# Kernel optimization log

Measured on AMD Instinct MI355X. Metric: run time of the kernel, lower is better.

The kernel has to match this reference:

```python
import jax, jax.numpy as jnp
import numpy as np

DIM = 2048
DIM_HEAD = 128
HEADS = 16
FF_MULT = 4
ATTN_INNER = DIM_HEAD * HEADS            # 2048
FF_INNER = DIM * FF_MULT                 # 8192
FUSED_OUT = ATTN_INNER + 2 * DIM_HEAD + 2 * FF_INNER  # 18688
EPS = 1e-5


def setup_inputs() -> dict:
    key = jax.random.key(0)
    ks = jax.random.split(key, 5)
    B, N = 1, 2048
    x = jax.random.normal(ks[0], (B, N, DIM), dtype=jnp.float32)
    gamma = jnp.ones((DIM,), dtype=jnp.float32)
    # store weights as [in, out] for x @ W
    w_fused = jax.random.normal(ks[1], (DIM, FUSED_OUT), dtype=jnp.float32) * (DIM ** -0.5)
    w_attn_out = jax.random.normal(ks[2], (ATTN_INNER, DIM), dtype=jnp.float32) * (ATTN_INNER ** -0.5)
    w_ff_out = jax.random.normal(ks[3], (FF_INNER, DIM), dtype=jnp.float32) * (FF_INNER ** -0.5)
    return {"x": x, "gamma": gamma, "w_fused": w_fused,
            "w_attn_out": w_attn_out, "w_ff_out": w_ff_out}


def reference(x, gamma, w_fused, w_attn_out, w_ff_out):
    b, n, d = x.shape
    h, dh = HEADS, DIM_HEAD
    scale = dh ** -0.5

    # LayerNorm (beta fixed at 0)
    mu = jnp.mean(x, axis=-1, keepdims=True)
    var = jnp.mean(jnp.square(x - mu), axis=-1, keepdims=True)
    xn = (x - mu) * jax.lax.rsqrt(var + EPS) * gamma

    # fused QKV + FF projection
    proj = xn @ w_fused  # [b, n, FUSED_OUT]
    q = proj[..., :ATTN_INNER]
    k = proj[..., ATTN_INNER:ATTN_INNER + dh]
    v = proj[..., ATTN_INNER + dh:ATTN_INNER + 2 * dh]
    ff = proj[..., ATTN_INNER + 2 * dh:]

    # multi-query attention: q per-head, k/v shared
    q = q.reshape(b, n, h, dh).transpose(0, 2, 1, 3) * scale  # [b,h,n,dh]
    sim = jnp.einsum('bhid,bjd->bhij', q, k)
    causal = jnp.triu(jnp.ones((n, n), dtype=bool), k=1)
    neg = -jnp.finfo(sim.dtype).max
    sim = jnp.where(causal, neg, sim)
    attn = jax.nn.softmax(sim, axis=-1)
    out = jnp.einsum('bhij,bjd->bhid', attn, v)
    out = out.transpose(0, 2, 1, 3).reshape(b, n, h * dh)
    attn_out = out @ w_attn_out

    # parallel SwiGLU FFN
    ff_x, gate = jnp.split(ff, 2, axis=-1)
    ff_out = (jax.nn.silu(gate) * ff_x) @ w_ff_out

    return attn_out + ff_out
```

## Files before the change

kernel.cpp:

```cpp
#include <hip/hip_runtime.h>
#include <hip/hip_bf16.h>

typedef unsigned short u16;
typedef __bf16 bf16x8 __attribute__((ext_vector_type(8)));
typedef float f32x4 __attribute__((ext_vector_type(4)));

#define DIM 2048
#define SEQ 2048
#define HEADS 16
#define DH 128
#define FUSED_OUT 18688
#define FF_INNER 8192
#define KOFF 2048
#define VOFF 2176
#define FFOFF 2304
#define AE_LD 10240

#define WS_XN   0
#define WS_WFT  8388608
#define WS_PROJ 84934656
#define WS_VT   161480704
#define WS_BTE  0
#define WS_AE   41943040

__device__ __forceinline__ float b2f(u16 u) {
  union { unsigned int i; float f; } c; c.i = ((unsigned int)u) << 16; return c.f;
}
__device__ __forceinline__ u16 f2b(float f) {
  union { float f; unsigned int i; } c; c.f = f;
  return (u16)((c.i + 0x7fffu + ((c.i >> 16) & 1u)) >> 16);
}
__device__ __forceinline__ void async16(void* lds, const void* g) {
  __builtin_amdgcn_global_load_lds((const __attribute__((address_space(1))) unsigned int*)g,
                                   (__attribute__((address_space(3))) unsigned int*)lds,
                                   16, 0, 0);
}

union U8 { uint4 v; u16 s[8]; };

__global__ void __launch_bounds__(256) ln_kernel(const float* __restrict__ x,
                                                 const float* __restrict__ gamma,
                                                 u16* __restrict__ xn) {
  const int row = blockIdx.x, tid = threadIdx.x;
  const int lane = tid & 63, wv = tid >> 6;
  float v[8], s1 = 0.f, s2 = 0.f;
  {
    float4 a0 = *(const float4*)(x + (size_t)row * DIM + tid * 8);
    float4 a1 = *(const float4*)(x + (size_t)row * DIM + tid * 8 + 4);
    v[0] = a0.x; v[1] = a0.y; v[2] = a0.z; v[3] = a0.w;
    v[4] = a1.x; v[5] = a1.y; v[6] = a1.z; v[7] = a1.w;
  }
#pragma unroll
  for (int i = 0; i < 8; ++i) { s1 += v[i]; s2 += v[i] * v[i]; }
#pragma unroll
  for (int off = 32; off > 0; off >>= 1) {
    s1 += __shfl_down(s1, off, 64);
    s2 += __shfl_down(s2, off, 64);
  }
  __shared__ float r1[4], r2[4];
  if (lane == 0) { r1[wv] = s1; r2[wv] = s2; }
  __syncthreads();
  s1 = r1[0] + r1[1] + r1[2] + r1[3];
  s2 = r2[0] + r2[1] + r2[2] + r2[3];
  const float inv = 1.0f / DIM;
  const float mu = s1 * inv;
  const float var = s2 * inv - mu * mu;
  const float rs = rsqrtf(var + 1e-5f);
  float4 g0 = *(const float4*)(gamma + tid * 8);
  float4 g1 = *(const float4*)(gamma + tid * 8 + 4);
  const float gm[8] = {g0.x, g0.y, g0.z, g0.w, g1.x, g1.y, g1.z, g1.w};
  U8 o;
#pragma unroll
  for (int i = 0; i < 8; ++i) o.s[i] = f2b((v[i] - mu) * rs * gm[i]);
  *(uint4*)(xn + (size_t)row * DIM + tid * 8) = o.v;
}

__global__ void __launch_bounds__(256) transpose_f2b64(const float* __restrict__ in,
                                                       u16* __restrict__ out,
                                                       int ldin, int ldout) {
  __shared__ u16 t[64][65];
  const int tx = threadIdx.x, ty = threadIdx.y;
  const int r0 = blockIdx.y * 64, c0 = blockIdx.x * 64;
#pragma unroll
  for (int i = 0; i < 16; ++i)
    t[ty + i * 4][tx] = f2b(in[(size_t)(r0 + ty + i * 4) * ldin + c0 + tx]);
  __syncthreads();
#pragma unroll
  for (int i = 0; i < 16; ++i)
    out[(size_t)(c0 + ty + i * 4) * ldout + r0 + tx] = t[tx][ty + i * 4];
}

__global__ void __launch_bounds__(256) trans_wout64(const float* __restrict__ w_attn,
                                                    const float* __restrict__ w_ff,
                                                    u16* __restrict__ BtE) {
  __shared__ u16 t[64][65];
  const int tx = threadIdx.x, ty = threadIdx.y;
  const int c0 = blockIdx.x * 64;
  const float* in; int r0, kout;
  if (blockIdx.y < 32) { in = w_attn; r0 = blockIdx.y * 64; kout = r0; }
  else { in = w_ff; r0 = (blockIdx.y - 32) * 64; kout = 2048 + r0; }
#pragma unroll
  for (int i = 0; i < 16; ++i)
    t[ty + i * 4][tx] = f2b(in[(size_t)(r0 + ty + i * 4) * DIM + c0 + tx]);
  __syncthreads();
#pragma unroll
  for (int i = 0; i < 16; ++i)
    BtE[(size_t)(c0 + ty + i * 4) * AE_LD + kout + tx] = t[tx][ty + i * 4];
}

__global__ void __launch_bounds__(256) transpose_u16_64(const u16* __restrict__ in,
                                                        u16* __restrict__ out,
                                                        int ldin, int ldout) {
  __shared__ u16 t[64][65];
  const int tx = threadIdx.x, ty = threadIdx.y;
  const int r0 = blockIdx.y * 64, c0 = blockIdx.x * 64;
#pragma unroll
  for (int i = 0; i < 16; ++i)
    t[ty + i * 4][tx] = in[(size_t)(r0 + ty + i * 4) * ldin + c0 + tx];
  __syncthreads();
#pragma unroll
  for (int i = 0; i < 16; ++i)
    out[(size_t)(c0 + ty + i * 4) * ldout + r0 + tx] = t[tx][ty + i * 4];
}

#define BAR()    asm volatile("s_barrier" ::: "memory")
#define LGKM0()  asm volatile("s_waitcnt lgkmcnt(0)" ::: "memory")
#define RA(mi, kk) (*(const bf16x8*)&sA[c][(wm * 128 + (mi) * 16 + lhalf) * 64 + ((((kk) * 4 + lgrp) ^ key) << 3)])
#define RB(ni, kk) (*(const bf16x8*)&sB[c][(wn * 64 + (ni) * 16 + lhalf) * 64 + ((((kk) * 4 + lgrp) ^ key) << 3)])
#define MFMA_Q(MB, AA)                                                   \
  _Pragma("unroll") for (int kk = 0; kk < 2; ++kk)                       \
  _Pragma("unroll") for (int u = 0; u < 2; ++u)                          \
  _Pragma("unroll") for (int ni = 0; ni < 4; ++ni)                       \
      acc[(MB) + u][ni] = __builtin_amdgcn_mfma_f32_16x16x32_bf16(       \
          AA[u][kk], bF[ni][kk], acc[(MB) + u][ni], 0, 0, 0);

__device__ __forceinline__ void stage_h(u16* lds, const u16* g, int ld,
                                        int wv, int srow, int scol) {
  async16(lds + wv * 512,        g + (size_t)(wv * 8 + srow) * ld + scol);
  async16(lds + 4096 + wv * 512, g + (size_t)(64 + wv * 8 + srow) * ld + scol);
}

template <int OUTMODE>
__global__ void __launch_bounds__(512, 2) gemm8p(const u16* __restrict__ A,
                                                 const u16* __restrict__ Bt,
                                                 void* __restrict__ Cv,
                                                 int Ksz, int lda, int ldb, int ldc) {
  __shared__ alignas(16) u16 sA[2][256 * 64];
  __shared__ alignas(16) u16 sB[2][256 * 64];
  const int tid = threadIdx.x;
  const int lane = tid & 63, wv = tid >> 6;
  const int wm = wv >> 2, wn = wv & 3;
  const int lhalf = lane & 15, lgrp = lane >> 4;
  const int key = lhalf & 7;
  const int srow = lane >> 3;
  const int scol = ((lane & 7) ^ srow) << 3;
  const int m0 = blockIdx.x * 256, n0 = blockIdx.y * 256;
  const int kbeg = blockIdx.z * Ksz;
  const int NT = Ksz >> 6;

  const u16* Abase = A + (size_t)m0 * lda + kbeg;
  const u16* Bbase = Bt + (size_t)n0 * ldb + kbeg;

  stage_h(&sB[0][0],    Bbase,                     ldb, wv, srow, scol);
  stage_h(&sB[0][8192], Bbase + (size_t)128 * ldb, ldb, wv, srow, scol);
  stage_h(&sA[0][0],    Abase,                     lda, wv, srow, scol);
  stage_h(&sA[0][8192], Abase + (size_t)128 * lda, lda, wv, srow, scol);
  asm volatile("s_waitcnt vmcnt(4)" ::: "memory");
  stage_h(&sB[1][0],    Bbase + 64,                     ldb, wv, srow, scol);
  stage_h(&sB[1][8192], Bbase + (size_t)128 * ldb + 64, ldb, wv, srow, scol);
  stage_h(&sA[1][0],    Abase + 64,                     lda, wv, srow, scol);
  asm volatile("s_waitcnt vmcnt(6)" ::: "memory");
  BAR();

  f32x4 acc[8][4];
  const f32x4 fzero = {0.f, 0.f, 0.f, 0.f};
#pragma unroll
  for (int i = 0; i < 8; ++i)
#pragma unroll
    for (int j = 0; j < 4; ++j) acc[i][j] = fzero;

  bf16x8 bF[4][2];
  bf16x8 aF[2][2];
  bf16x8 aX[2][2];

  int t1w = 1;
  int t2w = 2 % NT;
  for (int t = 0; t < NT; ++t) {
    const int c = t & 1;
#pragma unroll
    for (int kk = 0; kk < 2; ++kk) {
      aF[0][kk] = RA(0, kk); aF[1][kk] = RA(1, kk);
#pragma unroll
      for (int ni = 0; ni < 4; ++ni) bF[ni][kk] = RB(ni, kk);
    }
    stage_h(&sA[c ^ 1][8192], Abase + (size_t)128 * lda + t1w * 64, lda, wv, srow, scol);
    asm volatile("s_waitcnt lgkmcnt(8)" ::: "memory");
    BAR(); LGKM0();
    __builtin_amdgcn_s_setprio(1);
    MFMA_Q(0, aF);
    __builtin_amdgcn_s_setprio(0);
    BAR();
#pragma unroll
    for (int kk = 0; kk < 2; ++kk) { aF[0][kk] = RA(2, kk); aF[1][kk] = RA(3, kk); }
    stage_h(&sB[c][0], Bbase + t2w * 64, ldb, wv, srow, scol);
    BAR(); LGKM0();
    __builtin_amdgcn_s_setprio(1);
    MFMA_Q(2, aF);
    __builtin_amdgcn_s_setprio(0);
    BAR();
#pragma unroll
    for (int kk = 0; kk < 2; ++kk) { aF[0][kk] = RA(4, kk); aF[1][kk] = RA(5, kk); }
    if (wm == 0) {
#pragma unroll
      for (int kk = 0; kk < 2; ++kk) { aX[0][kk] = RA(6, kk); aX[1][kk] = RA(7, kk); }
    }
    stage_h(&sB[c][8192], Bbase + (size_t)128 * ldb + t2w * 64, ldb, wv, srow, scol);
    BAR(); LGKM0();
    __builtin_amdgcn_s_setprio(1);
    MFMA_Q(4, aF);
    __builtin_amdgcn_s_setprio(0);
    BAR();
    if (wm != 0) {
#pragma unroll
      for (int kk = 0; kk < 2; ++kk) { aF[0][kk] = RA(6, kk); aF[1][kk] = RA(7, kk); }
    }
    stage_h(&sA[c][0], Abase + t2w * 64, lda, wv, srow, scol);
    asm volatile("s_waitcnt vmcnt(6)" ::: "memory");
    BAR(); LGKM0();
    __builtin_amdgcn_s_setprio(1);
    if (wm == 0) { MFMA_Q(6, aX); } else { MFMA_Q(6, aF); }
    __builtin_amdgcn_s_setprio(0);
    BAR();
    t1w = (t1w + 1 == NT) ? 0 : t1w + 1;
    t2w = (t2w + 1 == NT) ? 0 : t2w + 1;
  }
  asm volatile("s_waitcnt vmcnt(0)" ::: "memory");
#pragma unroll
  for (int mi = 0; mi < 8; ++mi)
#pragma unroll
    for (int ni = 0; ni < 4; ++ni)
#pragma unroll
      for (int tt = 0; tt < 4; ++tt) {
        const int row = m0 + wm * 128 + mi * 16 + lgrp * 4 + tt;
        const int col = n0 + wn * 64 + ni * 16 + lhalf;
        if (OUTMODE == 0) ((u16*)Cv)[(size_t)row * ldc + col] = f2b(acc[mi][ni][tt]);
        else atomicAdd((float*)Cv + (size_t)row * ldc + col, acc[mi][ni][tt]);
      }
}

__global__ void __launch_bounds__(256) attn_kernel(const u16* __restrict__ proj,
                                                   const u16* __restrict__ Vt,
                                                   u16* __restrict__ Ae) {
  const int h = blockIdx.y, qi = blockIdx.x;
  const int tid = threadIdx.x;
  const int lane = tid & 63, wv = tid >> 6;
  const int lhalf = lane & 15, lgrp = lane >> 4;
  const int key = lhalf & 7;

  __shared__ alignas(16) u16 Ks[128 * 128];
  __shared__ alignas(16) u16 Vts[128 * 128];
  __shared__ alignas(16) u16 Ps[4][16 * 128];

  const int sr = lane >> 4;
  const int sb = lane & 15;

  bf16x8 aq[4];
  {
    const u16* gq = proj + (size_t)(qi * 64 + wv * 16 + lhalf) * FUSED_OUT + h * DH;
#pragma unroll
    for (int kk = 0; kk < 4; ++kk) aq[kk] = *(const bf16x8*)(gq + kk * 32 + lgrp * 8);
  }
  const f32x4 fzero = {0.f, 0.f, 0.f, 0.f};
  f32x4 o[8];
#pragma unroll
  for (int i = 0; i < 8; ++i) o[i] = fzero;
  float mrow[4] = {-__builtin_inff(), -__builtin_inff(), -__builtin_inff(), -__builtin_inff()};
  float lrow[4] = {0.f, 0.f, 0.f, 0.f};
  const float scale = 0.088388347648318447f;
  const int jmax = (qi * 64 + 63) >> 7;

  for (int jt = 0; jt <= jmax; ++jt) {
    __syncthreads();
#pragma unroll
    for (int i = 0; i < 8; ++i) {
      const int ch = wv * 8 + i;
      const int row = ch * 4 + sr;
      const int gb = sb ^ (row & 7);
      async16(&Ks[ch * 512], proj + (size_t)(jt * 128 + row) * FUSED_OUT + KOFF + gb * 8);
      async16(&Vts[ch * 512], Vt + (size_t)row * SEQ + jt * 128 + gb * 8);
    }
    __syncthreads();
    f32x4 s[8];
#pragma unroll
    for (int sub = 0; sub < 8; ++sub) {
      f32x4 a = fzero;
#pragma unroll
      for (int kk = 0; kk < 4; ++kk) {
        bf16x8 bk = *(const bf16x8*)&Ks[(sub * 16 + lhalf) * 128 + (((kk * 4 + lgrp) ^ key) << 3)];
        a = __builtin_amdgcn_mfma_f32_16x16x32_bf16(aq[kk], bk, a, 0, 0, 0);
      }
      s[sub] = a;
    }
    const int row_g = qi * 64 + wv * 16 + lgrp * 4;
    const int col_b = jt * 128 + lhalf;
#pragma unroll
    for (int t = 0; t < 4; ++t) {
      float mx = -__builtin_inff();
#pragma unroll
      for (int sub = 0; sub < 8; ++sub) {
        float v = s[sub][t] * scale;
        if (col_b + sub * 16 > row_g + t) v = -__builtin_inff();
        s[sub][t] = v;
        mx = fmaxf(mx, v);
      }
      mx = fmaxf(mx, __shfl_xor(mx, 1, 64));
      mx = fmaxf(mx, __shfl_xor(mx, 2, 64));
      mx = fmaxf(mx, __shfl_xor(mx, 4, 64));
      mx = fmaxf(mx, __shfl_xor(mx, 8, 64));
      const float mnew = fmaxf(mrow[t], mx);
      const float alpha = __expf(mrow[t] - mnew);
      mrow[t] = mnew;
      float ls = 0.f;
#pragma unroll
      for (int sub = 0; sub < 8; ++sub) {
        const float p = __expf(s[sub][t] - mnew);
        s[sub][t] = p;
        ls += p;
      }
      ls += __shfl_xor(ls, 1, 64);
      ls += __shfl_xor(ls, 2, 64);
      ls += __shfl_xor(ls, 4, 64);
      ls += __shfl_xor(ls, 8, 64);
      lrow[t] = lrow[t] * alpha + ls;
      const int prow = lgrp * 4 + t;
      const int pkey = prow & 7;
#pragma unroll
      for (int sub = 0; sub < 8; ++sub) {
        o[sub][t] *= alpha;
        const int b = sub * 2 + (lhalf >> 3);
        Ps[wv][prow * 128 + ((b ^ pkey) << 3) + (lhalf & 7)] = f2b(s[sub][t]);
      }
    }
    asm volatile("s_waitcnt lgkmcnt(0)" ::: "memory");
#pragma unroll
    for (int kk = 0; kk < 4; ++kk) {
      bf16x8 ap = *(const bf16x8*)&Ps[wv][lhalf * 128 + (((kk * 4 + lgrp) ^ key) << 3)];
#pragma unroll
      for (int sub = 0; sub < 8; ++sub) {
        bf16x8 bv = *(const bf16x8*)&Vts[(sub * 16 + lhalf) * 128 + (((kk * 4 + lgrp) ^ key) << 3)];
        o[sub] = __builtin_amdgcn_mfma_f32_16x16x32_bf16(ap, bv, o[sub], 0, 0, 0);
      }
    }
  }
#pragma unroll
  for (int sub = 0; sub < 8; ++sub)
#pragma unroll
    for (int t = 0; t < 4; ++t) {
      const int row = qi * 64 + wv * 16 + lgrp * 4 + t;
      const int col = h * DH + sub * 16 + lhalf;
      Ae[(size_t)row * AE_LD + col] = f2b(o[sub][t] / lrow[t]);
    }
}

__global__ void __launch_bounds__(256) ffa_kernel(const u16* __restrict__ proj,
                                                  u16* __restrict__ Ae) {
  const size_t idx = (size_t)blockIdx.x * 256 + threadIdx.x;
  const size_t e = idx * 8;
  const int row = (int)(e >> 13);
  const int j = (int)(e & 8191);
  const u16* base = proj + (size_t)row * FUSED_OUT + FFOFF;
  U8 xr, gr, os;
  xr.v = *(const uint4*)(base + j);
  gr.v = *(const uint4*)(base + FF_INNER + j);
#pragma unroll
  for (int i = 0; i < 8; ++i) {
    const float g = b2f(gr.s[i]);
    const float sg = g / (1.f + __expf(-g));
    os.s[i] = f2b(sg * b2f(xr.s[i]));
  }
  *(uint4*)(Ae + (size_t)row * AE_LD + 2048 + j) = os.v;
}

extern "C" void kernel_launch(void* const* d_in, const int* in_sizes, int n_in,
                              void* d_out, int out_size, void* d_ws, size_t ws_size,
                              hipStream_t stream) {
  const float* x       = (const float*)d_in[0];
  const float* gamma   = (const float*)d_in[1];
  const float* w_fused = (const float*)d_in[2];
  const float* w_attn  = (const float*)d_in[3];
  const float* w_ff    = (const float*)d_in[4];
  float* out = (float*)d_out;
  char* ws = (char*)d_ws;
  u16* xn   = (u16*)(ws + WS_XN);
  u16* wfT  = (u16*)(ws + WS_WFT);
  u16* proj = (u16*)(ws + WS_PROJ);
  u16* Vt   = (u16*)(ws + WS_VT);
  u16* BtE  = (u16*)(ws + WS_BTE);
  u16* Ae   = (u16*)(ws + WS_AE);

  hipMemsetAsync(d_out, 0, (size_t)out_size * sizeof(float), stream);

  ln_kernel<<<dim3(2048), dim3(256), 0, stream>>>(x, gamma, xn);
  transpose_f2b64<<<dim3(292, 32), dim3(64, 4), 0, stream>>>(w_fused, wfT, FUSED_OUT, DIM);
  gemm8p<0><<<dim3(8, 73, 1), dim3(512), 0, stream>>>(xn, wfT, proj, DIM, DIM, DIM, FUSED_OUT);

  transpose_u16_64<<<dim3(2, 32), dim3(64, 4), 0, stream>>>(proj + VOFF, Vt, FUSED_OUT, SEQ);
  trans_wout64<<<dim3(32, 160), dim3(64, 4), 0, stream>>>(w_attn, w_ff, BtE);
  attn_kernel<<<dim3(32, 16), dim3(256), 0, stream>>>(proj, Vt, Ae);
  ffa_kernel<<<dim3(8192), dim3(256), 0, stream>>>(proj, Ae);

  gemm8p<2><<<dim3(8, 8, 4), dim3(512), 0, stream>>>(Ae, BtE, out, AE_LD / 4, AE_LD, AE_LD, DIM);
}
```

Before: 745.1 us.

## Restructure GEMM main loop into k-split phases with quarter-tile staging and swizzled block order

Reorganizes the 256x256 bf16 GEMM inner loop so each phase issues 16 MFMAs over four M-subtiles for one k-half, instead of eight MFMAs over two k-halves. Global-to-LDS staging is split into quarter-tile async copies spread across the phases. Compiler sched_barriers are added so the compiler cannot move instructions across the phase boundaries. Block indices are also remapped so consecutive workgroups are spread across groups of eight (likely targeting XCD/L2 locality). The change aims at better overlap of loads with MFMA and better cache reuse, but raises register pressure and the remap assumes grid dimensions that are multiples of eight.

```diff
diff --git a/kernel.cpp b/kernel.cpp
--- a/kernel.cpp
+++ b/kernel.cpp
@@ -123,21 +123,20 @@
     out[(size_t)(c0 + ty + i * 4) * ldout + r0 + tx] = t[tx][ty + i * 4];
 }
 
-#define BAR()    asm volatile("s_barrier" ::: "memory")
+#define BAR()    __builtin_amdgcn_s_barrier()
 #define LGKM0()  asm volatile("s_waitcnt lgkmcnt(0)" ::: "memory")
-#define RA(mi, kk) (*(const bf16x8*)&sA[c][(wm * 128 + (mi) * 16 + lhalf) * 64 + ((((kk) * 4 + lgrp) ^ key) << 3)])
-#define RB(ni, kk) (*(const bf16x8*)&sB[c][(wn * 64 + (ni) * 16 + lhalf) * 64 + ((((kk) * 4 + lgrp) ^ key) << 3)])
-#define MFMA_Q(MB, AA)                                                   \
-  _Pragma("unroll") for (int kk = 0; kk < 2; ++kk)                       \
-  _Pragma("unroll") for (int u = 0; u < 2; ++u)                          \
+#define SCHED0() __builtin_amdgcn_sched_barrier(0)
+#define RA(mi, kk) (*(const bf16x8*)&pA[(wm * 128 + (mi) * 16 + lhalf) * 64 + ((((kk) * 4 + lgrp) ^ key) << 3)])
+#define RB(ni, kk) (*(const bf16x8*)&pB[(wn * 64 + (ni) * 16 + lhalf) * 64 + ((((kk) * 4 + lgrp) ^ key) << 3)])
+#define MFMA16(MB, KK, AA)                                               \
+  _Pragma("unroll") for (int u = 0; u < 4; ++u)                          \
   _Pragma("unroll") for (int ni = 0; ni < 4; ++ni)                       \
       acc[(MB) + u][ni] = __builtin_amdgcn_mfma_f32_16x16x32_bf16(       \
-          AA[u][kk], bF[ni][kk], acc[(MB) + u][ni], 0, 0, 0);
-
-__device__ __forceinline__ void stage_h(u16* lds, const u16* g, int ld,
+          AA[u], bF[KK][ni], acc[(MB) + u][ni], 0, 0, 0);
+
+__device__ __forceinline__ void stage_q(u16* lds, const u16* g, int ld,
                                         int wv, int srow, int scol) {
-  async16(lds + wv * 512,        g + (size_t)(wv * 8 + srow) * ld + scol);
-  async16(lds + 4096 + wv * 512, g + (size_t)(64 + wv * 8 + srow) * ld + scol);
+  async16(lds + wv * 512, g + (size_t)(wv * 8 + srow) * ld + scol);
 }
 
 template <int OUTMODE>
@@ -154,21 +153,30 @@
   const int key = lhalf & 7;
   const int srow = lane >> 3;
   const int scol = ((lane & 7) ^ srow) << 3;
-  const int m0 = blockIdx.x * 256, n0 = blockIdx.y * 256;
+  const int nxy = gridDim.x * gridDim.y;
+  const int wg = blockIdx.x + (blockIdx.y << 3);
+  const int orig = (wg & 7) * (nxy >> 3) + (wg >> 3);
+  const int m0 = (orig & 7) * 256, n0 = (orig >> 3) * 256;
   const int kbeg = blockIdx.z * Ksz;
   const int NT = Ksz >> 6;
 
   const u16* Abase = A + (size_t)m0 * lda + kbeg;
   const u16* Bbase = Bt + (size_t)n0 * ldb + kbeg;
 
-  stage_h(&sB[0][0],    Bbase,                     ldb, wv, srow, scol);
-  stage_h(&sB[0][8192], Bbase + (size_t)128 * ldb, ldb, wv, srow, scol);
-  stage_h(&sA[0][0],    Abase,                     lda, wv, srow, scol);
-  stage_h(&sA[0][8192], Abase + (size_t)128 * lda, lda, wv, srow, scol);
-  asm volatile("s_waitcnt vmcnt(4)" ::: "memory");
-  stage_h(&sB[1][0],    Bbase + 64,                     ldb, wv, srow, scol);
-  stage_h(&sB[1][8192], Bbase + (size_t)128 * ldb + 64, ldb, wv, srow, scol);
-  stage_h(&sA[1][0],    Abase + 64,                     lda, wv, srow, scol);
+  stage_q(&sB[0][0],     Bbase,                     ldb, wv, srow, scol);
+  stage_q(&sB[0][4096],  Bbase + (size_t)64 * ldb,  ldb, wv, srow, scol);
+  stage_q(&sB[0][8192],  Bbase + (size_t)128 * ldb, ldb, wv, srow, scol);
+  stage_q(&sB[0][12288], Bbase + (size_t)192 * ldb, ldb, wv, srow, scol);
+  stage_q(&sA[0][0],     Abase,                     lda, wv, srow, scol);
+  stage_q(&sA[0][4096],  Abase + (size_t)64 * lda,  lda, wv, srow, scol);
+  stage_q(&sA[0][8192],  Abase + (size_t)128 * lda, lda, wv, srow, scol);
+  stage_q(&sA[0][12288], Abase + (size_t)192 * lda, lda, wv, srow, scol);
+  stage_q(&sA[1][0],     Abase + 64,                     lda, wv, srow, scol);
+  stage_q(&sA[1][8192],  Abase + (size_t)128 * lda + 64, lda, wv, srow, scol);
+  stage_q(&sB[1][0],     Bbase + 64,                     ldb, wv, srow, scol);
+  stage_q(&sB[1][4096],  Bbase + (size_t)64 * ldb + 64,  ldb, wv, srow, scol);
+  stage_q(&sB[1][8192],  Bbase + (size_t)128 * ldb + 64, ldb, wv, srow, scol);
+  stage_q(&sB[1][12288], Bbase + (size_t)192 * ldb + 64, ldb, wv, srow, scol);
   asm volatile("s_waitcnt vmcnt(6)" ::: "memory");
   BAR();
 
@@ -179,58 +187,57 @@
 #pragma unroll
     for (int j = 0; j < 4; ++j) acc[i][j] = fzero;
 
-  bf16x8 bF[4][2];
-  bf16x8 aF[2][2];
-  bf16x8 aX[2][2];
+  bf16x8 bF[2][4];
+  bf16x8 aF0[4];
+  bf16x8 aF1[4];
 
   int t1w = 1;
   int t2w = 2 % NT;
   for (int t = 0; t < NT; ++t) {
     const int c = t & 1;
-#pragma unroll
-    for (int kk = 0; kk < 2; ++kk) {
-      aF[0][kk] = RA(0, kk); aF[1][kk] = RA(1, kk);
-#pragma unroll
-      for (int ni = 0; ni < 4; ++ni) bF[ni][kk] = RB(ni, kk);
-    }
-    stage_h(&sA[c ^ 1][8192], Abase + (size_t)128 * lda + t1w * 64, lda, wv, srow, scol);
-    asm volatile("s_waitcnt lgkmcnt(8)" ::: "memory");
-    BAR(); LGKM0();
+    const u16* pA = &sA[c][0];
+    const u16* pB = &sB[c][0];
+#pragma unroll
+    for (int ni = 0; ni < 4; ++ni) bF[0][ni] = RB(ni, 0);
+#pragma unroll
+    for (int u = 0; u < 4; ++u) aF0[u] = RA(u, 0);
+    stage_q(&sA[c ^ 1][4096],  Abase + (size_t)64 * lda + t1w * 64,  lda, wv, srow, scol);
+    stage_q(&sA[c ^ 1][12288], Abase + (size_t)192 * lda + t1w * 64, lda, wv, srow, scol);
+    BAR(); LGKM0(); SCHED0();
     __builtin_amdgcn_s_setprio(1);
-    MFMA_Q(0, aF);
+    MFMA16(0, 0, aF0);
     __builtin_amdgcn_s_setprio(0);
-    BAR();
-#pragma unroll
-    for (int kk = 0; kk < 2; ++kk) { aF[0][kk] = RA(2, kk); aF[1][kk] = RA(3, kk); }
-    stage_h(&sB[c][0], Bbase + t2w * 64, ldb, wv, srow, scol);
-    BAR(); LGKM0();
+    SCHED0(); BAR();
+#pragma unroll
+    for (int ni = 0; ni < 4; ++ni) bF[1][ni] = RB(ni, 1);
+#pragma unroll
+    for (int u = 0; u < 4; ++u) aF1[u] = RA(u, 1);
+    BAR(); LGKM0(); SCHED0();
     __builtin_amdgcn_s_setprio(1);
-    MFMA_Q(2, aF);
+    MFMA16(0, 1, aF1);
     __builtin_amdgcn_s_setprio(0);
-    BAR();
-#pragma unroll
-    for (int kk = 0; kk < 2; ++kk) { aF[0][kk] = RA(4, kk); aF[1][kk] = RA(5, kk); }
-    if (wm == 0) {
-#pragma unroll
-      for (int kk = 0; kk < 2; ++kk) { aX[0][kk] = RA(6, kk); aX[1][kk] = RA(7, kk); }
-    }
-    stage_h(&sB[c][8192], Bbase + (size_t)128 * ldb + t2w * 64, ldb, wv, srow, scol);
-    BAR(); LGKM0();
+    SCHED0(); BAR();
+#pragma unroll
+    for (int u = 0; u < 4; ++u) aF0[u] = RA(4 + u, 0);
+    stage_q(&sA[c][0],     Abase + t2w * 64,                     lda, wv, srow, scol);
+    stage_q(&sA[c][8192],  Abase + (size_t)128 * lda + t2w * 64, lda, wv, srow, scol);
+    stage_q(&sB[c][0],     Bbase + t2w * 64,                     ldb, wv, srow, scol);
+    stage_q(&sB[c][4096],  Bbase + (size_t)64 * ldb + t2w * 64,  ldb, wv, srow, scol);
+    BAR(); LGKM0(); SCHED0();
     __builtin_amdgcn_s_setprio(1);
-    MFMA_Q(4, aF);
+    MFMA16(4, 0, aF0);
     __builtin_amdgcn_s_setprio(0);
-    BAR();
-    if (wm != 0) {
-#pragma unroll
-      for (int kk = 0; kk < 2; ++kk) { aF[0][kk] = RA(6, kk); aF[1][kk] = RA(7, kk); }
-    }
-    stage_h(&sA[c][0], Abase + t2w * 64, lda, wv, srow, scol);
+    SCHED0(); BAR();
+#pragma unroll
+    for (int u = 0; u < 4; ++u) aF1[u] = RA(4 + u, 1);
+    stage_q(&sB[c][8192],  Bbase + (size_t)128 * ldb + t2w * 64, ldb, wv, srow, scol);
+    stage_q(&sB[c][12288], Bbase + (size_t)192 * ldb + t2w * 64, ldb, wv, srow, scol);
     asm volatile("s_waitcnt vmcnt(6)" ::: "memory");
-    BAR(); LGKM0();
+    BAR(); LGKM0(); SCHED0();
     __builtin_amdgcn_s_setprio(1);
-    if (wm == 0) { MFMA_Q(6, aX); } else { MFMA_Q(6, aF); }
+    MFMA16(4, 1, aF1);
     __builtin_amdgcn_s_setprio(0);
-    BAR();
+    SCHED0(); BAR();
     t1w = (t1w + 1 == NT) ? 0 : t1w + 1;
     t2w = (t2w + 1 == NT) ? 0 : t2w + 1;
   }
```

Measured after the change: 748.2 us. About the same (+0.4%).
